# Performance work log

Measured on AMD Instinct MI355X. Metric: run time of the kernel, lower is better.

## Reference

```python
import jax, jax.numpy as jnp
import numpy as np

B, H, NSTEPS = 4096, 1024, 10
T0, T1 = 0.0, 1.0


def setup_inputs() -> dict:
    key = jax.random.key(0)
    k0, k1, k2, k3 = jax.random.split(key, 4)
    s = 0.03  # keep tanh in active region
    return {
        "h0": jax.random.normal(k0, (B, H), dtype=jnp.float32),
        "W1": jax.random.normal(k1, (H + 1, 2 * H), dtype=jnp.float32) * s,
        "b1": jnp.zeros((2 * H,), dtype=jnp.float32),
        "W2": jax.random.normal(k2, (2 * H, 2 * H), dtype=jnp.float32) * s,
        "b2": jnp.zeros((2 * H,), dtype=jnp.float32),
        "W3": jax.random.normal(k3, (2 * H, H), dtype=jnp.float32) * s,
        "b3": jnp.zeros((H,), dtype=jnp.float32),
    }


def _ode_func(t, h, W1, b1, W2, b2, W3, b3):
    # time-dependent: append a column of t to the state  -> (B, H+1)
    tcol = jnp.full((h.shape[0], 1), t, dtype=h.dtype)
    x = jnp.concatenate([h, tcol], axis=1)
    x = jnp.tanh(x @ W1 + b1)
    x = jnp.tanh(x @ W2 + b2)
    return x @ W3 + b3  # (B, H)


def _integrate(h0, W1, b1, W2, b2, W3, b3):
    t = jnp.linspace(T0, T1, NSTEPS + 1, dtype=jnp.float32)
    dt = t[1:] - t[:-1]

    def f(ti, h):
        return _ode_func(ti, h, W1, b1, W2, b2, W3, b3)

    def step(h, td):
        ti, dti = td
        k1 = f(ti, h)
        k2 = f(ti + dti / 2, h + (dti / 2) * k1)
        k3 = f(ti + dti / 2, h + (dti / 2) * k2)
        k4 = f(ti + dti, h + dti * k3)
        h_next = h + (dti / 6) * (k1 + 2 * k2 + 2 * k3 + k4)
        return h_next, None

    h1, _ = jax.lax.scan(step, h0, (t[:-1], dt))
    return h1


def reference(h0, W1, b1, W2, b2, W3, b3):
    return _integrate(h0, W1, b1, W2, b2, W3, b3)
```

## Files before the change

### kernel.cpp

```cpp
#include <hip/hip_runtime.h>
#include <cstdint>
#include <cstddef>

typedef _Float16 half8 __attribute__((ext_vector_type(8)));
typedef float floatx4 __attribute__((ext_vector_type(4)));

typedef __attribute__((address_space(3))) unsigned lds_u32;
typedef const __attribute__((address_space(1))) unsigned glb_u32;

#define BK 64

__device__ __forceinline__ void glds16(const void* g, void* l) {
    __builtin_amdgcn_global_load_lds((glb_u32*)g, (lds_u32*)l, 16, 0, 0);
}

__device__ __forceinline__ float fast_tanh(float x) {
    float ax = fabsf(x);
    float e  = __expf(-2.0f * ax);
    float t  = (1.0f - e) / (1.0f + e);
    return x < 0.0f ? -t : t;
}

template <int MT, int NT, int NPX>
__device__ __forceinline__ void map_block(int id, int& mt, int& nt) {
    constexpr int NG  = NT / NPX;
    constexpr int XPG = 8 / NG;
    const int xcd  = id & 7;
    const int slot = id >> 3;
    nt = (xcd % NG) * NPX + (slot % NPX);
    mt = (xcd / NG) * (MT / XPG) + slot / NPX;
}

template <int TBM, int TBN, int MF, int NF, int NW>
__device__ __forceinline__ void gemm_acc_db(const _Float16* __restrict__ A,
                                            const _Float16* __restrict__ BT,
                                            unsigned m0, unsigned n0,
                                            int K, floatx4 acc[MF][NF]) {
    constexpr int CW = TBN / (16 * NF);
    constexpr int RW = TBM / (16 * MF);
    static_assert(RW * CW == NW, "wave grid must use all waves");
    constexpr int AH  = TBM * 32;
    constexpr int BH  = TBN * 32;
    constexpr int NCA = TBM / 16;
    constexpr int NCB = TBN / 16;
    constexpr int UA  = (NCA + NW - 1) / NW;
    constexpr int UB  = (NCB + NW - 1) / NW;

    __shared__ __align__(16) _Float16 As[2][TBM * BK];
    __shared__ __align__(16) _Float16 Bs[2][TBN * BK];

    const int tid  = threadIdx.x;
    const int lane = tid & 63;
    const int wid  = tid >> 6;

    const int srow = lane >> 2;
    const int skq  = (lane & 3) ^ ((lane >> 3) & 3);
    const int quad = lane >> 4;
    const int l16  = lane & 15;
    const int wm   = (wid / CW) * (16 * MF);
    const int wn   = (wid % CW) * (16 * NF);

    const unsigned kstr = (unsigned)K * 2u;
    const unsigned aB0  = (m0 + (unsigned)srow) * kstr + (unsigned)(skq * 16);
    const unsigned bB0  = (n0 + (unsigned)srow) * kstr + (unsigned)(skq * 16);
    const char* Abase = (const char*)A;
    const char* Bbase = (const char*)BT;

#pragma unroll
    for (int i = 0; i < MF; ++i)
#pragma unroll
        for (int j = 0; j < NF; ++j)
            acc[i][j] = 0.0f;

    auto stage = [&](int buf, unsigned kb) {
#pragma unroll
        for (int h = 0; h < 2; ++h) {
#pragma unroll
            for (int u = 0; u < UA; ++u) {
                const int c = wid + u * NW;
                if ((NCA % NW == 0) || c < NCA)
                    glds16(Abase + (aB0 + (unsigned)c * (16u * kstr) + kb + (unsigned)(h * 64)),
                           &As[buf][h * AH + c * 512]);
            }
#pragma unroll
            for (int u = 0; u < UB; ++u) {
                const int c = wid + u * NW;
                if ((NCB % NW == 0) || c < NCB)
                    glds16(Bbase + (bB0 + (unsigned)c * (16u * kstr) + kb + (unsigned)(h * 64)),
                           &Bs[buf][h * BH + c * 512]);
            }
        }
    };

    const int rdoff = l16 * 32 + ((quad ^ ((l16 >> 1) & 3)) << 3);
    const unsigned Kb = (unsigned)K * 2u;
    const unsigned BKb = BK * 2u;

    stage(0, 0);
    int cur = 0;
    for (unsigned kb = 0; kb < Kb; kb += BKb) {
        __syncthreads();
        if (kb + BKb < Kb) stage(cur ^ 1, kb + BKb);

#pragma unroll
        for (int h = 0; h < 2; ++h) {
            half8 av[MF], bv[NF];
#pragma unroll
            for (int i = 0; i < MF; ++i)
                av[i] = *(const half8*)(&As[cur][h * AH + ((wm >> 4) + i) * 512 + rdoff]);
#pragma unroll
            for (int j = 0; j < NF; ++j)
                bv[j] = *(const half8*)(&Bs[cur][h * BH + ((wn >> 4) + j) * 512 + rdoff]);
#pragma unroll
            for (int i = 0; i < MF; ++i)
#pragma unroll
                for (int j = 0; j < NF; ++j)
                    acc[i][j] = __builtin_amdgcn_mfma_f32_16x16x32_f16(av[i], bv[j], acc[i][j], 0, 0, 0);
        }
        cur ^= 1;
    }
}


template <bool WITH_T, int MT, int NT>
__global__ __launch_bounds__(512)
void gemm_bias_tanh(const _Float16* __restrict__ A, const _Float16* __restrict__ BT,
                    _Float16* __restrict__ out, const float* __restrict__ bias,
                    const float* __restrict__ brow, float t, int N, int K) {
    int mt, nt;
    map_block<MT, NT, 4>(blockIdx.x, mt, nt);
    const unsigned bm0 = (unsigned)mt * 128;
    const unsigned bn0 = (unsigned)nt * 128;

    floatx4 acc[4][2];
    gemm_acc_db<128, 128, 4, 2, 8>(A, BT, bm0, bn0, K, acc);

    const int tid  = threadIdx.x;
    const int lane = tid & 63;
    const int wid  = tid >> 6;
    const int quad = lane >> 4;
    const int l16  = lane & 15;
    const size_t m0 = bm0 + (size_t)(wid / 4) * 64;
    const size_t n0 = bn0 + (size_t)(wid % 4) * 32;

#pragma unroll
    for (int j = 0; j < 2; ++j) {
        const size_t col = n0 + j * 16 + l16;
        float b = bias[col];
        if (WITH_T) b += t * brow[col];
#pragma unroll
        for (int i = 0; i < 4; ++i) {
            const size_t rbase = m0 + i * 16 + quad * 4;
#pragma unroll
            for (int r = 0; r < 4; ++r) {
                out[(rbase + r) * (size_t)N + col] = (_Float16)fast_tanh(acc[i][j][r] + b);
            }
        }
    }
}

__global__ __launch_bounds__(512)
void gemm_k_stage(const _Float16* __restrict__ A, const _Float16* __restrict__ BT,
                  const float* __restrict__ bias, float* __restrict__ hstate,
                  const _Float16* __restrict__ h16r, _Float16* __restrict__ h16w,
                  _Float16* __restrict__ accb, _Float16* __restrict__ x,
                  int stage, float c, float dt6, int N, int K) {
    int mt, nt;
    map_block<64, 8, 2>(blockIdx.x, mt, nt);
    const unsigned bm0 = (unsigned)mt * 64;
    const unsigned bn0 = (unsigned)nt * 128;

    floatx4 acc[2][2];
    gemm_acc_db<64, 128, 2, 2, 8>(A, BT, bm0, bn0, K, acc);

    const int tid  = threadIdx.x;
    const int lane = tid & 63;
    const int wid  = tid >> 6;
    const int quad = lane >> 4;
    const int l16  = lane & 15;
    const size_t m0 = bm0 + (size_t)(wid / 4) * 32;
    const size_t n0 = bn0 + (size_t)(wid % 4) * 32;

#pragma unroll
    for (int j = 0; j < 2; ++j) {
        const size_t col = n0 + j * 16 + l16;
        const float b = bias[col];
#pragma unroll
        for (int i = 0; i < 2; ++i) {
            const size_t rbase = m0 + i * 16 + quad * 4;
#pragma unroll
            for (int r = 0; r < 4; ++r) {
                const size_t idx = (rbase + r) * (size_t)N + col;
                const float k = acc[i][j][r] + b;
                if (stage == 0) {
                    accb[idx] = (_Float16)k;
                    x[idx] = (_Float16)((float)h16r[idx] + c * k);
                } else if (stage < 3) {
                    accb[idx] = (_Float16)((float)accb[idx] + 2.0f * k);
                    x[idx] = (_Float16)((float)h16r[idx] + c * k);
                } else {
                    const float hn = hstate[idx] + dt6 * ((float)accb[idx] + k);
                    hstate[idx] = hn;
                    h16w[idx] = (_Float16)hn;
                }
            }
        }
    }
}

__global__ __launch_bounds__(256)
void transposeW(const float* __restrict__ W, _Float16* __restrict__ WT,
                int K, int N) {
    __shared__ float tile[32][33];
    const int tx = threadIdx.x;
    const int ty = threadIdx.y;
    const int n0 = blockIdx.x * 32;
    const int k0 = blockIdx.y * 32;
#pragma unroll
    for (int r = ty; r < 32; r += 8)
        tile[r][tx] = W[(size_t)(k0 + r) * N + n0 + tx];
    __syncthreads();
#pragma unroll
    for (int r = ty; r < 32; r += 8)
        WT[(size_t)(n0 + r) * K + k0 + tx] = (_Float16)tile[tx][r];
}

__global__ void copy_row(const float* __restrict__ W1, float* __restrict__ w1row, int N) {
    const int n = blockIdx.x * 256 + threadIdx.x;
    if (n < N) w1row[n] = W1[(size_t)1024 * N + n];
}

__global__ void init_h(const float* __restrict__ h0, float* __restrict__ hstate,
                       _Float16* __restrict__ h16, int n) {
    const int i = blockIdx.x * 256 + threadIdx.x;
    if (i < n) {
        const float v = h0[i];
        hstate[i] = v;
        h16[i] = (_Float16)v;
    }
}

extern "C" void kernel_launch(void* const* d_in, const int* in_sizes, int n_in,
                              void* d_out, int out_size, void* d_ws, size_t ws_size,
                              hipStream_t stream) {
    const int B = 4096, H = 1024, H2 = 2048;

    const float* h0 = (const float*)d_in[0];
    const float* W1 = (const float*)d_in[1];
    const float* b1 = (const float*)d_in[2];
    const float* W2 = (const float*)d_in[3];
    const float* b2 = (const float*)d_in[4];
    const float* W3 = (const float*)d_in[5];
    const float* b3 = (const float*)d_in[6];

    float* hstate = (float*)d_out;

    char* ws = (char*)d_ws;
    _Float16* x    = (_Float16*)ws; ws += (size_t)B * H  * 2;
    _Float16* h16  = (_Float16*)ws; ws += (size_t)B * H  * 2;
    _Float16* a1   = (_Float16*)ws; ws += (size_t)B * H2 * 2;
    _Float16* a2   = (_Float16*)ws; ws += (size_t)B * H2 * 2;
    _Float16* accb = (_Float16*)ws; ws += (size_t)B * H  * 2;
    _Float16* W1T  = (_Float16*)ws; ws += (size_t)H2 * H  * 2;
    _Float16* W2T  = (_Float16*)ws; ws += (size_t)H2 * H2 * 2;
    _Float16* W3T  = (_Float16*)ws; ws += (size_t)H  * H2 * 2;
    float*   w1row = (float*)ws;    ws += (size_t)H2 * 4;

    const dim3 tblk(32, 8);
    transposeW<<<dim3(H2 / 32, H  / 32), tblk, 0, stream>>>(W1, W1T, H,  H2);
    transposeW<<<dim3(H2 / 32, H2 / 32), tblk, 0, stream>>>(W2, W2T, H2, H2);
    transposeW<<<dim3(H  / 32, H2 / 32), tblk, 0, stream>>>(W3, W3T, H2, H);
    copy_row<<<dim3(H2 / 256), 256, 0, stream>>>(W1, w1row, H2);
    init_h<<<dim3((B * H + 255) / 256), 256, 0, stream>>>(h0, hstate, h16, B * H);

    const float dt  = 0.1f;
    const float dt2 = 0.05f;
    const float dt6 = dt / 6.0f;

    const dim3 blk(512);
    const int g12 = (B / 128) * (H2 / 128);
    const int g3  = (B / 64) * (H / 128);

    for (int s = 0; s < 10; ++s) {
        const float ti = (float)s * dt;

        gemm_bias_tanh<true , 32, 16><<<g12, blk, 0, stream>>>(h16, W1T, a1, b1, w1row, ti,       H2, H);
        gemm_bias_tanh<false, 32, 16><<<g12, blk, 0, stream>>>(a1,  W2T, a2, b2, nullptr, 0.f,    H2, H2);
        gemm_k_stage<<<g3, blk, 0, stream>>>(a2, W3T, b3, hstate, h16, h16, accb, x, 0, dt2, dt6, H, H2);

        gemm_bias_tanh<true , 32, 16><<<g12, blk, 0, stream>>>(x,  W1T, a1, b1, w1row, ti + dt2, H2, H);
        gemm_bias_tanh<false, 32, 16><<<g12, blk, 0, stream>>>(a1, W2T, a2, b2, nullptr, 0.f,    H2, H2);
        gemm_k_stage<<<g3, blk, 0, stream>>>(a2, W3T, b3, hstate, h16, h16, accb, x, 1, dt2, dt6, H, H2);

        gemm_bias_tanh<true , 32, 16><<<g12, blk, 0, stream>>>(x,  W1T, a1, b1, w1row, ti + dt2, H2, H);
        gemm_bias_tanh<false, 32, 16><<<g12, blk, 0, stream>>>(a1, W2T, a2, b2, nullptr, 0.f,    H2, H2);
        gemm_k_stage<<<g3, blk, 0, stream>>>(a2, W3T, b3, hstate, h16, h16, accb, x, 2, dt,  dt6, H, H2);

        gemm_bias_tanh<true , 32, 16><<<g12, blk, 0, stream>>>(x,  W1T, a1, b1, w1row, ti + dt,  H2, H);
        gemm_bias_tanh<false, 32, 16><<<g12, blk, 0, stream>>>(a1, W2T, a2, b2, nullptr, 0.f,    H2, H2);
        gemm_k_stage<<<g3, blk, 0, stream>>>(a2, W3T, b3, hstate, h16, h16, accb, x, 3, dt,  dt6, H, H2);
    }
}
```

Before: 4.129 ms.

## Replace first two GEMM kernels with 256x128-tile, 4-stage pipelined kernel

Introduces a new GEMM+bias+tanh kernel with a larger 256x128 block tile and a 4-slot LDS ring of 32-wide K chunks. Loads are issued three stages ahead with explicit vmcnt waits and barriers, and MFMA sections run at raised wave priority. Each wave now computes a 4x4 fragment grid for more reuse per LDS read. The aim is to hide global-load latency and raise MFMA utilisation in the two large GEMMs. In exchange it uses more LDS and registers, and there are half as many blocks to fill the GPU.

```diff
diff --git a/kernel.cpp b/kernel.cpp
--- a/kernel.cpp
+++ b/kernel.cpp
@@ -13,6 +13,19 @@
 __device__ __forceinline__ void glds16(const void* g, void* l) {
     __builtin_amdgcn_global_load_lds((glb_u32*)g, (lds_u32*)l, 16, 0, 0);
 }
+
+template <int N>
+__device__ __forceinline__ void waitv() {
+    asm volatile("s_waitcnt vmcnt(%0)" :: "n"(N) : "memory");
+}
+
+__device__ __forceinline__ void barfence() {
+    asm volatile("" ::: "memory");
+    __builtin_amdgcn_s_barrier();
+    asm volatile("" ::: "memory");
+}
+
+template <int N> struct IC { static constexpr int value = N; };
 
 __device__ __forceinline__ float fast_tanh(float x) {
     float ax = fabsf(x);
@@ -29,6 +42,107 @@
     const int slot = id >> 3;
     nt = (xcd % NG) * NPX + (slot % NPX);
     mt = (xcd / NG) * (MT / XPG) + slot / NPX;
+}
+
+template <bool WITH_T>
+__global__ __launch_bounds__(512, 2)
+void gemm_bias_tanh_p8(const _Float16* __restrict__ A, const _Float16* __restrict__ BT,
+                       _Float16* __restrict__ out, const float* __restrict__ bias,
+                       const float* __restrict__ brow, float t, int N, int K) {
+    int mt, nt;
+    map_block<16, 16, 4>(blockIdx.x, mt, nt);
+    const unsigned bm0 = (unsigned)mt * 256;
+    const unsigned bn0 = (unsigned)nt * 128;
+
+    __shared__ __align__(16) _Float16 As[4][256 * 32];
+    __shared__ __align__(16) _Float16 Bs[4][128 * 32];
+
+    const int tid  = threadIdx.x;
+    const int lane = tid & 63;
+    const int wid  = tid >> 6;
+    const int srow = lane >> 2;
+    const int skq  = (lane & 3) ^ ((lane >> 3) & 3);
+    const int quad = lane >> 4;
+    const int l16  = lane & 15;
+    const int wmc  = (wid >> 1) * 4;
+    const int wnc  = (wid & 1) * 4;
+    const int rdoff = l16 * 32 + ((quad ^ ((l16 >> 1) & 3)) << 3);
+
+    const unsigned kstr = (unsigned)K * 2u;
+    const unsigned aB0  = (bm0 + (unsigned)srow) * kstr + (unsigned)(skq * 16);
+    const unsigned bB0  = (bn0 + (unsigned)srow) * kstr + (unsigned)(skq * 16);
+    const char* Abase = (const char*)A;
+    const char* Bbase = (const char*)BT;
+
+    floatx4 acc[4][4];
+#pragma unroll
+    for (int i = 0; i < 4; ++i)
+#pragma unroll
+        for (int j = 0; j < 4; ++j)
+            acc[i][j] = 0.0f;
+
+    auto stageS = [&](int s) {
+        const unsigned kb   = (unsigned)s * 64u;
+        const int      slot = s & 3;
+        glds16(Abase + (aB0 + (unsigned)wid       * (16u * kstr) + kb),
+               &As[slot][wid * 512]);
+        glds16(Abase + (aB0 + (unsigned)(wid + 8) * (16u * kstr) + kb),
+               &As[slot][(wid + 8) * 512]);
+        glds16(Bbase + (bB0 + (unsigned)wid       * (16u * kstr) + kb),
+               &Bs[slot][wid * 512]);
+    };
+
+    auto phase = [&](int s, auto dc) {
+        constexpr int D = decltype(dc)::value;
+        const int slot = s & 3;
+        half8 av[4], bv[4];
+#pragma unroll
+        for (int i = 0; i < 4; ++i)
+            av[i] = *(const half8*)(&As[slot][(wmc + i) * 512 + rdoff]);
+#pragma unroll
+        for (int j = 0; j < 4; ++j)
+            bv[j] = *(const half8*)(&Bs[slot][(wnc + j) * 512 + rdoff]);
+        if constexpr (D == 3) stageS(s + 3);
+        if constexpr (D >= 1) waitv<(D - 1) * 3>();
+        barfence();
+        asm volatile("s_waitcnt lgkmcnt(0)" ::: "memory");
+        __builtin_amdgcn_s_setprio(1);
+#pragma unroll
+        for (int i = 0; i < 4; ++i)
+#pragma unroll
+            for (int j = 0; j < 4; ++j)
+                acc[i][j] = __builtin_amdgcn_mfma_f32_16x16x32_f16(av[i], bv[j], acc[i][j], 0, 0, 0);
+        __builtin_amdgcn_s_setprio(0);
+        barfence();
+    };
+
+    stageS(0); stageS(1); stageS(2);
+    waitv<6>();
+    barfence();
+
+    const int NP = K >> 5;
+    int s = 0;
+    for (; s + 3 < NP; ++s) phase(s, IC<3>{});
+    phase(s, IC<2>{}); ++s;
+    phase(s, IC<1>{}); ++s;
+    phase(s, IC<0>{});
+
+    const size_t m0 = bm0 + (size_t)(wid >> 1) * 64;
+    const size_t n0 = bn0 + (size_t)(wid & 1) * 64;
+#pragma unroll
+    for (int j = 0; j < 4; ++j) {
+        const size_t col = n0 + j * 16 + l16;
+        float b = bias[col];
+        if (WITH_T) b += t * brow[col];
+#pragma unroll
+        for (int i = 0; i < 4; ++i) {
+            const size_t rbase = m0 + i * 16 + quad * 4;
+#pragma unroll
+            for (int r = 0; r < 4; ++r) {
+                out[(rbase + r) * (size_t)N + col] = (_Float16)fast_tanh(acc[i][j][r] + b);
+            }
+        }
+    }
 }
 
 template <int TBM, int TBN, int MF, int NF, int NW>
@@ -118,44 +232,6 @@
                     acc[i][j] = __builtin_amdgcn_mfma_f32_16x16x32_f16(av[i], bv[j], acc[i][j], 0, 0, 0);
         }
         cur ^= 1;
-    }
-}
-
-
-template <bool WITH_T, int MT, int NT>
-__global__ __launch_bounds__(512)
-void gemm_bias_tanh(const _Float16* __restrict__ A, const _Float16* __restrict__ BT,
-                    _Float16* __restrict__ out, const float* __restrict__ bias,
-                    const float* __restrict__ brow, float t, int N, int K) {
-    int mt, nt;
-    map_block<MT, NT, 4>(blockIdx.x, mt, nt);
-    const unsigned bm0 = (unsigned)mt * 128;
-    const unsigned bn0 = (unsigned)nt * 128;
-
-    floatx4 acc[4][2];
-    gemm_acc_db<128, 128, 4, 2, 8>(A, BT, bm0, bn0, K, acc);
-
-    const int tid  = threadIdx.x;
-    const int lane = tid & 63;
-    const int wid  = tid >> 6;
-    const int quad = lane >> 4;
-    const int l16  = lane & 15;
-    const size_t m0 = bm0 + (size_t)(wid / 4) * 64;
-    const size_t n0 = bn0 + (size_t)(wid % 4) * 32;
-
-#pragma unroll
-    for (int j = 0; j < 2; ++j) {
-        const size_t col = n0 + j * 16 + l16;
-        float b = bias[col];
-        if (WITH_T) b += t * brow[col];
-#pragma unroll
-        for (int i = 0; i < 4; ++i) {
-            const size_t rbase = m0 + i * 16 + quad * 4;
-#pragma unroll
-            for (int r = 0; r < 4; ++r) {
-                out[(rbase + r) * (size_t)N + col] = (_Float16)fast_tanh(acc[i][j][r] + b);
-            }
-        }
     }
 }
 
@@ -278,26 +354,26 @@
     const float dt6 = dt / 6.0f;
 
     const dim3 blk(512);
-    const int g12 = (B / 128) * (H2 / 128);
+    const int g12 = (B / 256) * (H2 / 128);
     const int g3  = (B / 64) * (H / 128);
 
     for (int s = 0; s < 10; ++s) {
         const float ti = (float)s * dt;
 
-        gemm_bias_tanh<true , 32, 16><<<g12, blk, 0, stream>>>(h16, W1T, a1, b1, w1row, ti,       H2, H);
-        gemm_bias_tanh<false, 32, 16><<<g12, blk, 0, stream>>>(a1,  W2T, a2, b2, nullptr, 0.f,    H2, H2);
+        gemm_bias_tanh_p8<true ><<<g12, blk, 0, stream>>>(h16, W1T, a1, b1, w1row, ti,       H2, H);
+        gemm_bias_tanh_p8<false><<<g12, blk, 0, stream>>>(a1,  W2T, a2, b2, nullptr, 0.f,    H2, H2);
         gemm_k_stage<<<g3, blk, 0, stream>>>(a2, W3T, b3, hstate, h16, h16, accb, x, 0, dt2, dt6, H, H2);
 
-        gemm_bias_tanh<true , 32, 16><<<g12, blk, 0, stream>>>(x,  W1T, a1, b1, w1row, ti + dt2, H2, H);
-        gemm_bias_tanh<false, 32, 16><<<g12, blk, 0, stream>>>(a1, W2T, a2, b2, nullptr, 0.f,    H2, H2);
+        gemm_bias_tanh_p8<true ><<<g12, blk, 0, stream>>>(x,  W1T, a1, b1, w1row, ti + dt2, H2, H);
+        gemm_bias_tanh_p8<false><<<g12, blk, 0, stream>>>(a1, W2T, a2, b2, nullptr, 0.f,    H2, H2);
         gemm_k_stage<<<g3, blk, 0, stream>>>(a2, W3T, b3, hstate, h16, h16, accb, x, 1, dt2, dt6, H, H2);
 
-        gemm_bias_tanh<true , 32, 16><<<g12, blk, 0, stream>>>(x,  W1T, a1, b1, w1row, ti + dt2, H2, H);
-        gemm_bias_tanh<false, 32, 16><<<g12, blk, 0, stream>>>(a1, W2T, a2, b2, nullptr, 0.f,    H2, H2);
+        gemm_bias_tanh_p8<true ><<<g12, blk, 0, stream>>>(x,  W1T, a1, b1, w1row, ti + dt2, H2, H);
+        gemm_bias_tanh_p8<false><<<g12, blk, 0, stream>>>(a1, W2T, a2, b2, nullptr, 0.f,    H2, H2);
         gemm_k_stage<<<g3, blk, 0, stream>>>(a2, W3T, b3, hstate, h16, h16, accb, x, 2, dt,  dt6, H, H2);
 
-        gemm_bias_tanh<true , 32, 16><<<g12, blk, 0, stream>>>(x,  W1T, a1, b1, w1row, ti + dt,  H2, H);
-        gemm_bias_tanh<false, 32, 16><<<g12, blk, 0, stream>>>(a1, W2T, a2, b2, nullptr, 0.f,    H2, H2);
+        gemm_bias_tanh_p8<true ><<<g12, blk, 0, stream>>>(x,  W1T, a1, b1, w1row, ti + dt,  H2, H);
+        gemm_bias_tanh_p8<false><<<g12, blk, 0, stream>>>(a1, W2T, a2, b2, nullptr, 0.f,    H2, H2);
         gemm_k_stage<<<g3, blk, 0, stream>>>(a2, W3T, b3, hstate, h16, h16, accb, x, 3, dt,  dt6, H, H2);
     }
 }
```

New measurement: 4.308 ms. +4.3%, slower.
